# Kernel optimization log

Hardware: AMD Instinct MI355X
Metric: run time of the kernel (lower is better)

The kernel has to match this reference:

```python
import jax, jax.numpy as jnp
import numpy as np

N, D = 512, 64          # n_objects, object_dim
HG, OG = 256, 256       # g hidden, g output
HF, OF = 256, 64        # f hidden, f output


def setup_inputs() -> dict:
    key = jax.random.key(0)
    ks = jax.random.split(key, 16)
    s = 0.05
    inp = {
        "x": jax.random.normal(ks[0], (N, D), dtype=jnp.float32),
        "q": jax.random.normal(ks[1], (D,), dtype=jnp.float32),
        # MLP g: input 3*D -> HG -> OG (ReLU after every layer, nonlinear=True)
        "g_w1": jax.random.normal(ks[2], (3 * D, HG), dtype=jnp.float32) * s,
        "g_b1": jnp.zeros((HG,), dtype=jnp.float32),
        "g_w2": jax.random.normal(ks[3], (HG, OG), dtype=jnp.float32) * s,
        "g_b2": jnp.zeros((OG,), dtype=jnp.float32),
        # query_expand: D -> HG -> OG (nonlinear=True)
        "qe_w1": jax.random.normal(ks[4], (D, HG), dtype=jnp.float32) * s,
        "qe_b1": jnp.zeros((HG,), dtype=jnp.float32),
        "qe_w2": jax.random.normal(ks[5], (HG, OG), dtype=jnp.float32) * s,
        "qe_b2": jnp.zeros((OG,), dtype=jnp.float32),
        # MLP f: OG -> HF -> OF (ReLU on hidden only, nonlinear=False)
        "f_w1": jax.random.normal(ks[6], (OG, HF), dtype=jnp.float32) * s,
        "f_b1": jnp.zeros((HF,), dtype=jnp.float32),
        "f_w2": jax.random.normal(ks[7], (HF, OF), dtype=jnp.float32) * s,
        "f_b2": jnp.zeros((OF,), dtype=jnp.float32),
    }
    return inp


def reference(x, q, g_w1, g_b1, g_w2, g_b2, qe_w1, qe_b1, qe_w2, qe_b2,
              f_w1, f_b1, f_w2, f_b2):
    n, d = x.shape
    # pair (a,b): first half x_i = x[b], second half x_j = x[a], then query q
    xi = jnp.broadcast_to(x[None, :, :], (n, n, d))   # repeats x along dim 0
    xj = jnp.broadcast_to(x[:, None, :], (n, n, d))   # repeats x along dim 1
    qb = jnp.broadcast_to(q[None, None, :], (n, n, d))
    pair_concat = jnp.concatenate([xi, xj, qb], axis=-1).reshape(n * n, 3 * d)
    # g MLP (ReLU after every layer since nonlinear=True)
    h = jax.nn.relu(pair_concat @ g_w1 + g_b1)
    relations = jax.nn.relu(h @ g_w2 + g_b2)          # [N*N, OG]
    # attentional weighting
    qh = jax.nn.relu(q @ qe_w1 + qe_b1)
    q_exp = jax.nn.relu(qh @ qe_w2 + qe_b2)           # [OG]
    c = jax.nn.softmax(relations @ q_exp, axis=0)     # [N*N]
    embedding = jnp.sum(relations * c[:, None], axis=0)  # [OG]
    # f MLP (no final nonlinearity)
    fh = jax.nn.relu(embedding @ f_w1 + f_b1)
    out = fh @ f_w2 + f_b2                            # [OF]
    return out
```

## Files before the change

kernel.cpp:

```cpp
#include <hip/hip_runtime.h>
#include <hip/hip_bf16.h>

typedef __attribute__((ext_vector_type(8))) short s16x8;
typedef __attribute__((ext_vector_type(4))) float f32x4;

#define NSLOT 128

__device__ __forceinline__ short f2bf(float f) {
    union { float f; unsigned u; } c; c.f = f;
    unsigned u = c.u;
    return (short)((u + 0x7fffu + ((u >> 16) & 1u)) >> 16);
}

__global__ __launch_bounds__(256) void rn_k1(
    const float* __restrict__ x, const float* __restrict__ q,
    const float* __restrict__ g_w1, const float* __restrict__ g_b1,
    const float* __restrict__ g_w2,
    const float* __restrict__ qe_w1, const float* __restrict__ qe_b1,
    const float* __restrict__ qe_w2, const float* __restrict__ qe_b2,
    float* __restrict__ U, float* __restrict__ V,
    float* __restrict__ c0, float* __restrict__ qexp,
    short* __restrict__ w2s, float* __restrict__ accb)
{
    __shared__ float sbuf[64];
    __shared__ float qh[256];
    const int blk = blockIdx.x, t = threadIdx.x;

    if (blk < 512) {
        if (t < 64) sbuf[t] = x[blk * 64 + t];
        __syncthreads();
        float u = 0.f, v = 0.f;
        #pragma unroll 4
        for (int k = 0; k < 64; ++k) {
            float xv = sbuf[k];
            u += xv * g_w1[k * 256 + t];
            v += xv * g_w1[(64 + k) * 256 + t];
        }
        U[blk * 256 + t] = u;
        V[blk * 256 + t] = v;
        {
            int E = blk * 256 + t;
            int e = E & 7, f = E >> 3;
            int lane = f & 63, n = (f >> 6) & 3, kk = (f >> 8) & 7, wv = (f >> 11) & 3;
            int l15 = lane & 15, g = lane >> 4;
            int col = wv * 64 + n * 16 + l15;
            int k = kk * 32 + g * 8 + e;
            w2s[E] = f2bf(g_w2[k * 256 + col]);
        }
    } else if (blk == 512) {
        if (t < 64) sbuf[t] = q[t];
        __syncthreads();
        float cc = g_b1[t], hh = qe_b1[t];
        #pragma unroll 4
        for (int k = 0; k < 64; ++k) {
            float qv = sbuf[k];
            cc += qv * g_w1[(128 + k) * 256 + t];
            hh += qv * qe_w1[k * 256 + t];
        }
        c0[t] = cc;
        qh[t] = fmaxf(hh, 0.f);
        __syncthreads();
        float qe = qe_b2[t];
        #pragma unroll 4
        for (int k = 0; k < 256; ++k) qe += qh[k] * qe_w2[k * 256 + t];
        qexp[t] = fmaxf(qe, 0.f);
    } else {
        const int total = NSLOT * 257;
        int off = (blk - 513) * 2048 + t * 8;
        #pragma unroll
        for (int i = 0; i < 8; ++i)
            if (off + i < total) accb[off + i] = 0.f;
    }
}

__global__ __launch_bounds__(256, 4) void rn_k2(
    const float* __restrict__ U, const float* __restrict__ V,
    const float* __restrict__ c0, const float* __restrict__ qexp,
    const short* __restrict__ w2s, const float* __restrict__ g_b2,
    float* __restrict__ accb)
{
    __shared__ short hT[64][264];
    __shared__ float srowT[64][4];

    const int bid = blockIdx.x;
    const int a   = bid >> 3;
    const int b0  = (bid & 7) << 6;
    const int tid = threadIdx.x;
    const int wave = tid >> 6, lane = tid & 63;
    const int l15 = lane & 15, g = lane >> 4;
    const int col0 = wave << 6;

    {
        const int c4 = tid & 63;
        const int r0 = tid >> 6;
        const float4 vv  = *(const float4*)&V[a * 256 + c4 * 4];
        const float4 cc  = *(const float4*)&c0[c4 * 4];
        const float4 vcv = make_float4(vv.x + cc.x, vv.y + cc.y,
                                       vv.z + cc.z, vv.w + cc.w);
        #pragma unroll
        for (int it = 0; it < 16; ++it) {
            int row = r0 + it * 4;
            float4 uu = *(const float4*)&U[(b0 + row) * 256 + c4 * 4];
            __hip_bfloat162 p0 = __float22bfloat162_rn(
                make_float2(fmaxf(uu.x + vcv.x, 0.f), fmaxf(uu.y + vcv.y, 0.f)));
            __hip_bfloat162 p1 = __float22bfloat162_rn(
                make_float2(fmaxf(uu.z + vcv.z, 0.f), fmaxf(uu.w + vcv.w, 0.f)));
            uint2 st;
            st.x = *reinterpret_cast<unsigned*>(&p0);
            st.y = *reinterpret_cast<unsigned*>(&p1);
            *reinterpret_cast<uint2*>(&hT[row][c4 * 4]) = st;
        }
    }

    float qe[4], b2c[4];
    #pragma unroll
    for (int n = 0; n < 4; ++n) {
        int col = col0 + n * 16 + l15;
        qe[n]  = qexp[col];
        b2c[n] = g_b2[col];
    }
    __syncthreads();

    f32x4 acc[4][4];
    #pragma unroll
    for (int m = 0; m < 4; ++m)
        #pragma unroll
        for (int n = 0; n < 4; ++n)
            acc[m][n] = (f32x4){0.f, 0.f, 0.f, 0.f};

    #pragma unroll
    for (int kk = 0; kk < 8; ++kk) {
        const int koff = kk * 32 + g * 8;
        s16x8 bfr[4];
        #pragma unroll
        for (int n = 0; n < 4; ++n)
            bfr[n] = *(const s16x8*)&w2s[(((wave * 8 + kk) * 4 + n) * 64 + lane) * 8];
        s16x8 afr[4];
        #pragma unroll
        for (int m = 0; m < 4; ++m)
            afr[m] = *(const s16x8*)&hT[m * 16 + l15][koff];
        #pragma unroll
        for (int m = 0; m < 4; ++m)
            #pragma unroll
            for (int n = 0; n < 4; ++n)
                acc[m][n] = __builtin_amdgcn_mfma_f32_16x16x32_bf16(
                    afr[m], bfr[n], acc[m][n], 0, 0, 0);
    }

    #pragma unroll
    for (int m = 0; m < 4; ++m)
        #pragma unroll
        for (int n = 0; n < 4; ++n)
            #pragma unroll
            for (int j = 0; j < 4; ++j)
                acc[m][n][j] = fmaxf(acc[m][n][j] + b2c[n], 0.f);

    #pragma unroll
    for (int m = 0; m < 4; ++m) {
        #pragma unroll
        for (int j = 0; j < 4; ++j) {
            float sp = 0.f;
            #pragma unroll
            for (int n = 0; n < 4; ++n) sp += acc[m][n][j] * qe[n];
            sp += __shfl_xor(sp, 1);
            sp += __shfl_xor(sp, 2);
            sp += __shfl_xor(sp, 4);
            sp += __shfl_xor(sp, 8);
            if (l15 == 0) srowT[m * 16 + g * 4 + j][wave] = sp;
        }
    }
    __syncthreads();

    float wrow[4][4];
    #pragma unroll
    for (int m = 0; m < 4; ++m)
        #pragma unroll
        for (int j = 0; j < 4; ++j) {
            const float4 s4 = *(const float4*)&srowT[m * 16 + g * 4 + j][0];
            wrow[m][j] = __expf(s4.x + s4.y + s4.z + s4.w);
        }

    const int slot = bid & (NSLOT - 1);
    if (wave == 0) {
        float ls = 0.f;
        #pragma unroll
        for (int m = 0; m < 4; ++m)
            #pragma unroll
            for (int j = 0; j < 4; ++j) ls += wrow[m][j];
        ls += __shfl_xor(ls, 16);
        ls += __shfl_xor(ls, 32);
        if (lane == 0) atomicAdd(&accb[slot * 257 + 256], ls);
    }

    #pragma unroll
    for (int n = 0; n < 4; ++n) {
        float wv = 0.f;
        #pragma unroll
        for (int m = 0; m < 4; ++m)
            #pragma unroll
            for (int j = 0; j < 4; ++j)
                wv += wrow[m][j] * acc[m][n][j];
        wv += __shfl_xor(wv, 16);
        wv += __shfl_xor(wv, 32);
        if (lane < 16) atomicAdd(&accb[slot * 257 + col0 + n * 16 + lane], wv);
    }
}

__global__ __launch_bounds__(256) void rn_k4(
    const float* __restrict__ accb,
    const float* __restrict__ f_w1, const float* __restrict__ f_b1,
    const float* __restrict__ f_w2, const float* __restrict__ f_b2,
    float* __restrict__ out)
{
    __shared__ float emb[256];
    __shared__ float fh[256];
    const int t = threadIdx.x;

    float v = 0.f, ls = 0.f;
    #pragma unroll 8
    for (int s = 0; s < NSLOT; ++s) {
        v  += accb[s * 257 + t];
        ls += accb[s * 257 + 256];
    }
    emb[t] = v / ls;
    __syncthreads();

    float h = f_b1[t];
    #pragma unroll 4
    for (int k = 0; k < 256; ++k) h += emb[k] * f_w1[k * 256 + t];
    fh[t] = fmaxf(h, 0.f);
    __syncthreads();

    if (t < 64) {
        float o = f_b2[t];
        #pragma unroll 4
        for (int k = 0; k < 256; ++k) o += fh[k] * f_w2[k * 64 + t];
        out[t] = o;
    }
}

extern "C" void kernel_launch(void* const* d_in, const int* in_sizes, int n_in,
                              void* d_out, int out_size, void* d_ws, size_t ws_size,
                              hipStream_t stream) {
    const float* x     = (const float*)d_in[0];
    const float* q     = (const float*)d_in[1];
    const float* g_w1  = (const float*)d_in[2];
    const float* g_b1  = (const float*)d_in[3];
    const float* g_w2  = (const float*)d_in[4];
    const float* g_b2  = (const float*)d_in[5];
    const float* qe_w1 = (const float*)d_in[6];
    const float* qe_b1 = (const float*)d_in[7];
    const float* qe_w2 = (const float*)d_in[8];
    const float* qe_b2 = (const float*)d_in[9];
    const float* f_w1  = (const float*)d_in[10];
    const float* f_b1  = (const float*)d_in[11];
    const float* f_w2  = (const float*)d_in[12];
    const float* f_b2  = (const float*)d_in[13];

    float* wsf  = (float*)d_ws;
    float* U    = wsf;
    float* V    = wsf + 131072;
    float* c0   = wsf + 262144;
    float* qexp = wsf + 262400;
    short* w2s  = (short*)(wsf + 262656);
    float* accb = wsf + 328192;

    hipLaunchKernelGGL(rn_k1, dim3(530), dim3(256), 0, stream,
                       x, q, g_w1, g_b1, g_w2, qe_w1, qe_b1, qe_w2, qe_b2,
                       U, V, c0, qexp, w2s, accb);
    hipLaunchKernelGGL(rn_k2, dim3(4096), dim3(256), 0, stream,
                       U, V, c0, qexp, (const short*)w2s, g_b2, accb);
    hipLaunchKernelGGL(rn_k4, dim3(1), dim3(256), 0, stream,
                       accb, f_w1, f_b1, f_w2, f_b2, (float*)d_out);
}
```

Measured before the change: 83.06 us.

## Double-buffer MFMA operand loads in rn_k2 and split accumulators in rn_k4

In rn_k2 the LDS A-fragments and global W2 B-fragments are now software-pipelined with two register buffers, so the loads for step kk+1 are issued before the MFMAs of step kk. The first W2 loads and the qexp/bias loads are hoisted above the hT staging so their latency overlaps that work. Launch bounds drop from 4 to 3 waves per SIMD to leave room for the extra registers. rn_k4 uses four independent accumulators in its reduction and matvec loops to shorten the dependency chains. The cost is higher register pressure and possibly lower occupancy in rn_k2.

```diff
diff --git a/kernel.cpp b/kernel.cpp
--- a/kernel.cpp
+++ b/kernel.cpp
@@ -73,7 +73,7 @@
     }
 }
 
-__global__ __launch_bounds__(256, 4) void rn_k2(
+__global__ __launch_bounds__(256, 3) void rn_k2(
     const float* __restrict__ U, const float* __restrict__ V,
     const float* __restrict__ c0, const float* __restrict__ qexp,
     const short* __restrict__ w2s, const float* __restrict__ g_b2,
@@ -89,6 +89,21 @@
     const int wave = tid >> 6, lane = tid & 63;
     const int l15 = lane & 15, g = lane >> 4;
     const int col0 = wave << 6;
+
+    const short* w2w = w2s + (wave << 14);
+#define BFR_LOAD(kk, n) (*(const s16x8*)&w2w[(((kk) * 4 + (n)) << 9) + (lane << 3)])
+
+    s16x8 bfr[2][4];
+    #pragma unroll
+    for (int n = 0; n < 4; ++n) bfr[0][n] = BFR_LOAD(0, n);
+
+    float qe[4], b2c[4];
+    #pragma unroll
+    for (int n = 0; n < 4; ++n) {
+        int col = col0 + n * 16 + l15;
+        qe[n]  = qexp[col];
+        b2c[n] = g_b2[col];
+    }
 
     {
         const int c4 = tid & 63;
@@ -111,14 +126,6 @@
             *reinterpret_cast<uint2*>(&hT[row][c4 * 4]) = st;
         }
     }
-
-    float qe[4], b2c[4];
-    #pragma unroll
-    for (int n = 0; n < 4; ++n) {
-        int col = col0 + n * 16 + l15;
-        qe[n]  = qexp[col];
-        b2c[n] = g_b2[col];
-    }
     __syncthreads();
 
     f32x4 acc[4][4];
@@ -128,24 +135,31 @@
         for (int n = 0; n < 4; ++n)
             acc[m][n] = (f32x4){0.f, 0.f, 0.f, 0.f};
 
+    s16x8 afr[2][4];
+    #pragma unroll
+    for (int m = 0; m < 4; ++m)
+        afr[0][m] = *(const s16x8*)&hT[m * 16 + l15][g * 8];
+
     #pragma unroll
     for (int kk = 0; kk < 8; ++kk) {
-        const int koff = kk * 32 + g * 8;
-        s16x8 bfr[4];
+        const int cur = kk & 1, nxt = cur ^ 1;
+        if (kk < 7) {
+            const int koff = (kk + 1) * 32 + g * 8;
+            #pragma unroll
+            for (int m = 0; m < 4; ++m)
+                afr[nxt][m] = *(const s16x8*)&hT[m * 16 + l15][koff];
+            #pragma unroll
+            for (int n = 0; n < 4; ++n)
+                bfr[nxt][n] = BFR_LOAD(kk + 1, n);
+        }
         #pragma unroll
         for (int n = 0; n < 4; ++n)
-            bfr[n] = *(const s16x8*)&w2s[(((wave * 8 + kk) * 4 + n) * 64 + lane) * 8];
-        s16x8 afr[4];
-        #pragma unroll
-        for (int m = 0; m < 4; ++m)
-            afr[m] = *(const s16x8*)&hT[m * 16 + l15][koff];
-        #pragma unroll
-        for (int m = 0; m < 4; ++m)
-            #pragma unroll
-            for (int n = 0; n < 4; ++n)
+            #pragma unroll
+            for (int m = 0; m < 4; ++m)
                 acc[m][n] = __builtin_amdgcn_mfma_f32_16x16x32_bf16(
-                    afr[m], bfr[n], acc[m][n], 0, 0, 0);
-    }
+                    afr[cur][m], bfr[cur][n], acc[m][n], 0, 0, 0);
+    }
+#undef BFR_LOAD
 
     #pragma unroll
     for (int m = 0; m < 4; ++m)
@@ -216,26 +230,41 @@
     __shared__ float fh[256];
     const int t = threadIdx.x;
 
-    float v = 0.f, ls = 0.f;
+    float v0 = 0.f, v1 = 0.f, v2 = 0.f, v3 = 0.f;
+    float ls = 0.f;
+    #pragma unroll
+    for (int s = 0; s < NSLOT; s += 4) {
+        v0 += accb[(s + 0) * 257 + t];
+        v1 += accb[(s + 1) * 257 + t];
+        v2 += accb[(s + 2) * 257 + t];
+        v3 += accb[(s + 3) * 257 + t];
+        ls += accb[s * 257 + 256] + accb[(s + 1) * 257 + 256]
+            + accb[(s + 2) * 257 + 256] + accb[(s + 3) * 257 + 256];
+    }
+    emb[t] = (v0 + v1 + v2 + v3) / ls;
+    __syncthreads();
+
+    float h0 = f_b1[t], h1 = 0.f, h2 = 0.f, h3 = 0.f;
     #pragma unroll 8
-    for (int s = 0; s < NSLOT; ++s) {
-        v  += accb[s * 257 + t];
-        ls += accb[s * 257 + 256];
-    }
-    emb[t] = v / ls;
+    for (int k = 0; k < 256; k += 4) {
+        h0 += emb[k + 0] * f_w1[(k + 0) * 256 + t];
+        h1 += emb[k + 1] * f_w1[(k + 1) * 256 + t];
+        h2 += emb[k + 2] * f_w1[(k + 2) * 256 + t];
+        h3 += emb[k + 3] * f_w1[(k + 3) * 256 + t];
+    }
+    fh[t] = fmaxf((h0 + h1) + (h2 + h3), 0.f);
     __syncthreads();
 
-    float h = f_b1[t];
-    #pragma unroll 4
-    for (int k = 0; k < 256; ++k) h += emb[k] * f_w1[k * 256 + t];
-    fh[t] = fmaxf(h, 0.f);
-    __syncthreads();
-
     if (t < 64) {
-        float o = f_b2[t];
-        #pragma unroll 4
-        for (int k = 0; k < 256; ++k) o += fh[k] * f_w2[k * 64 + t];
-        out[t] = o;
+        float o0 = f_b2[t], o1 = 0.f, o2 = 0.f, o3 = 0.f;
+        #pragma unroll 8
+        for (int k = 0; k < 256; k += 4) {
+            o0 += fh[k + 0] * f_w2[(k + 0) * 64 + t];
+            o1 += fh[k + 1] * f_w2[(k + 1) * 64 + t];
+            o2 += fh[k + 2] * f_w2[(k + 2) * 64 + t];
+            o3 += fh[k + 3] * f_w2[(k + 3) * 64 + t];
+        }
+        out[t] = (o0 + o1) + (o2 + o3);
     }
 }
 
```

Measured after the change: 74.71 us. 10.1% less time.
